# Kernel optimization log

Hardware: AMD Instinct MI355X
Metric: run time of the kernel (lower is better)

The kernel has to match this reference:

```python
import jax, jax.numpy as jnp
import numpy as np

H = 16  # num_heads
THETA = 10000.0


def apply_rope(x, positions, theta=THETA):
    # x: [..., S, d_k]; positions: [S]
    d_k = x.shape[-1]
    inv_freq = theta ** (-jnp.arange(0, d_k, 2, dtype=jnp.float32) / d_k)  # [d_k/2]
    ang = positions.astype(jnp.float32)[:, None] * inv_freq[None, :]  # [S, d_k/2]
    cos, sin = jnp.cos(ang), jnp.sin(ang)
    x1 = x[..., 0::2]
    x2 = x[..., 1::2]
    out_even = x1 * cos - x2 * sin
    out_odd = x1 * sin + x2 * cos
    out = jnp.stack([out_even, out_odd], axis=-1)  # [..., S, d_k/2, 2]
    return out.reshape(x.shape)


def setup_inputs() -> dict:
    key = jax.random.key(0)
    k1, k2, k3 = jax.random.split(key, 3)
    B, S, D = 2, 2048, 1024
    x = jax.random.normal(k1, (B, S, D), dtype=jnp.float32)
    token_positions = jnp.arange(S, dtype=jnp.int32)
    w_qkv = jax.random.normal(k2, (3 * D, D), dtype=jnp.float32) * (D ** -0.5)
    w_out = jax.random.normal(k3, (D, D), dtype=jnp.float32) * (D ** -0.5)
    return {"x": x, "token_positions": token_positions, "w_qkv": w_qkv, "w_out": w_out}


def reference(x, token_positions, w_qkv, w_out):
    B, S, D = x.shape
    d_k = D // H
    qkv = jnp.einsum('bsd,ed->bse', x, w_qkv)  # [B,S,3D]
    # split '(n h d_k)' -> n=3, h=H, d_k
    qkv = qkv.reshape(B, S, 3, H, d_k).transpose(2, 0, 3, 1, 4)  # [3,B,H,S,d_k]
    q = apply_rope(qkv[0], token_positions)
    k = apply_rope(qkv[1], token_positions)
    v = qkv[2]
    scale = 1.0 / jnp.sqrt(jnp.asarray(d_k, dtype=x.dtype))
    scores = jnp.einsum('bhqd,bhkd->bhqk', q, k) * scale  # [B,H,S,S]
    causal = jnp.tril(jnp.ones((S, S), dtype=bool))
    scores = jnp.where(causal, scores, jnp.asarray(-1e30, dtype=scores.dtype))
    attn = jax.nn.softmax(scores, axis=-1)
    out = jnp.einsum('bhqk,bhkd->bhqd', attn, v)  # [B,H,S,d_k]
    out = out.transpose(0, 2, 1, 3).reshape(B, S, D)  # merge (h d_v)
    return jnp.einsum('bsd,ed->bse', out, w_out)
```

## Files before the change

### kernel.cpp

```cpp
#include <hip/hip_runtime.h>

using bf16 = __bf16;
typedef __bf16 bf16x2 __attribute__((ext_vector_type(2)));
typedef __bf16 bf16x4v __attribute__((ext_vector_type(4)));
typedef __bf16 bf16x8 __attribute__((ext_vector_type(8)));
typedef float f32x4 __attribute__((ext_vector_type(4)));
typedef float floatx4 __attribute__((ext_vector_type(4)));

#define MFMA16(a, b, c) __builtin_amdgcn_mfma_f32_16x16x32_bf16((a), (b), (c), 0, 0, 0)

__device__ __forceinline__ float exp2a(float x) {
  float r;
  asm("v_exp_f32 %0, %1" : "=v"(r) : "v"(x));
  return r;
}

__global__ __launch_bounds__(256) void cast_kernel(const float* __restrict__ in,
                                                   bf16* __restrict__ out, int n4) {
  int i = blockIdx.x * 256 + threadIdx.x;
  if (i >= n4) return;
  floatx4 v = *(const floatx4*)(in + (size_t)i * 4);
  bf16x4v o;
  #pragma unroll
  for (int j = 0; j < 4; ++j) o[j] = (bf16)v[j];
  *(bf16x4v*)(out + (size_t)i * 4) = o;
}

template <bool OUT_F32>
__global__ __launch_bounds__(256, 2) void gemm_bt(const bf16* __restrict__ A,
                                                  const bf16* __restrict__ B,
                                                  void* __restrict__ Cv,
                                                  int M, int N, int K) {
  __shared__ bf16 As[128 * 32];
  __shared__ bf16 Bs[128 * 32];
  const int t = threadIdx.x;
  const int l = t & 63;
  const int w = t >> 6;
  const int m0 = blockIdx.y * 128;
  const int n0 = blockIdx.x * 128;
  const int wr = (w >> 1) * 64;
  const int wc = (w & 1) * 64;
  const int lr = l & 15;
  const int lk = (l >> 4) * 8;

  f32x4 acc[4][4] = {};

  const int srow = t >> 2;
  const int scol = (t & 3) * 8;

  for (int k0 = 0; k0 < K; k0 += 32) {
    __syncthreads();
    #pragma unroll
    for (int j = 0; j < 2; ++j) {
      const bf16* ga = A + (size_t)(m0 + j * 64 + srow) * K + k0 + scol;
      __builtin_amdgcn_global_load_lds(
          (const __attribute__((address_space(1))) void*)ga,
          (__attribute__((address_space(3))) void*)(As + (j * 64 + srow) * 32 + scol),
          16, 0, 0);
      const bf16* gb = B + (size_t)(n0 + j * 64 + srow) * K + k0 + scol;
      __builtin_amdgcn_global_load_lds(
          (const __attribute__((address_space(1))) void*)gb,
          (__attribute__((address_space(3))) void*)(Bs + (j * 64 + srow) * 32 + scol),
          16, 0, 0);
    }
    __syncthreads();
    bf16x8 af[4], bfr[4];
    #pragma unroll
    for (int i = 0; i < 4; ++i) af[i] = *(const bf16x8*)(As + (wr + i * 16 + lr) * 32 + lk);
    #pragma unroll
    for (int i = 0; i < 4; ++i) bfr[i] = *(const bf16x8*)(Bs + (wc + i * 16 + lr) * 32 + lk);
    #pragma unroll
    for (int i = 0; i < 4; ++i)
      #pragma unroll
      for (int j = 0; j < 4; ++j)
        acc[i][j] = MFMA16(af[i], bfr[j], acc[i][j]);
  }

  const int cr0 = (l >> 4) * 4;
  const int cc = l & 15;
  #pragma unroll
  for (int i = 0; i < 4; ++i) {
    #pragma unroll
    for (int j = 0; j < 4; ++j) {
      int row = m0 + wr + i * 16 + cr0;
      int col = n0 + wc + j * 16 + cc;
      #pragma unroll
      for (int r = 0; r < 4; ++r) {
        if constexpr (OUT_F32)
          ((float*)Cv)[(size_t)(row + r) * N + col] = acc[i][j][r];
        else
          ((bf16*)Cv)[(size_t)(row + r) * N + col] = (bf16)acc[i][j][r];
      }
    }
  }
}

__global__ __launch_bounds__(256) void rope_kernel(bf16* __restrict__ qkv,
                                                   const int* __restrict__ pos) {
  int idx = blockIdx.x * 256 + threadIdx.x;
  int i = idx & 31;
  int h = (idx >> 5) & 15;
  int row = idx >> 9;
  int s = row & 2047;
  float p = (float)pos[s];
  float freq = exp2f(-(float)i * (13.287712379549449f / 32.0f));
  float ang = p * freq;
  float sn, cs;
  sincosf(ang, &sn, &cs);
  size_t base = (size_t)row * 3072 + h * 64 + 2 * i;
  bf16x2 q = *(bf16x2*)(qkv + base);
  bf16x2 k = *(bf16x2*)(qkv + base + 1024);
  float q1 = (float)q[0], q2 = (float)q[1];
  float k1 = (float)k[0], k2 = (float)k[1];
  bf16x2 qo, ko;
  qo[0] = (bf16)(q1 * cs - q2 * sn);
  qo[1] = (bf16)(q1 * sn + q2 * cs);
  ko[0] = (bf16)(k1 * cs - k2 * sn);
  ko[1] = (bf16)(k1 * sn + k2 * cs);
  *(bf16x2*)(qkv + base) = qo;
  *(bf16x2*)(qkv + base + 1024) = ko;
}

__global__ __launch_bounds__(256, 4) void fa_causal(const bf16* __restrict__ qkv,
                                                    bf16* __restrict__ attn) {
  const int bh = blockIdx.x;
  const int b = bh >> 4, h = bh & 15;
  const int q0 = ((int)gridDim.y - 1 - (int)blockIdx.y) * 64;
  const int t = threadIdx.x, w = t >> 6, l = t & 63;
  const int lq = l & 15;
  const int g = l >> 4;
  const int lk = g * 8;
  const int swz = lq & 7;
  const int hz = lq >> 3;

  __shared__ bf16 Ks[2][64 * 64];
  __shared__ bf16 Vt[2][64 * 64];

  const size_t rs = 3072;
  const bf16* Qg = qkv + (size_t)(b * 2048) * rs + h * 64;
  const bf16* Kg = Qg + 1024;
  const bf16* Vg = Qg + 2048;

  const int qrow0 = q0 + w * 16;
  const int qg = qrow0 + lq;

  const float SC = 0.125f * 1.44269504088896f;
  bf16x8 qfr[2];
  #pragma unroll
  for (int kk = 0; kk < 2; ++kk) {
    bf16x8 qv = *(const bf16x8*)(Qg + (size_t)qg * rs + kk * 32 + lk);
    #pragma unroll
    for (int j = 0; j < 8; ++j) qv[j] = (bf16)((float)qv[j] * SC);
    qfr[kk] = qv;
  }

  f32x4 o[4] = {};
  float mrow = -1e30f, lrow = 0.f;

  const int nkt = (q0 + 64) >> 6;
  const int krow_in = l >> 3;
  const int kcsrc = (l & 7) ^ krow_in;
  const int kp = t >> 3;
  const int K0 = kp * 2;
  const int cd = t & 7;
  const int slot0 = (K0 & 32) | (((K0 >> 2) & 3) << 3) | (((K0 >> 4) & 1) << 2) | (K0 & 3);

  bf16x8 va, vb2;

  #define STAGE_K(KT, BUF)                                                                \
    {                                                                                     \
      _Pragma("unroll")                                                                   \
      for (int c = 0; c < 2; ++c) {                                                       \
        const int rowbase = w * 8 + c * 32;                                               \
        const bf16* src = Kg + (size_t)((KT)*64 + rowbase + krow_in) * rs + kcsrc * 8;    \
        __builtin_amdgcn_global_load_lds(                                                 \
            (const __attribute__((address_space(1))) void*)src,                           \
            (__attribute__((address_space(3))) void*)(&Ks[BUF][rowbase * 64]), 16, 0, 0); \
      }                                                                                   \
    }
  #define LOAD_V(KT)                                                          \
    {                                                                         \
      const bf16* vsrc = Vg + (size_t)((KT)*64 + K0) * rs + cd * 8;           \
      va = *(const bf16x8*)(vsrc);                                            \
      vb2 = *(const bf16x8*)(vsrc + rs);                                      \
    }
  #define WRITE_V(BUF)                                                        \
    {                                                                         \
      _Pragma("unroll")                                                       \
      for (int e = 0; e < 8; ++e) {                                           \
        bf16x2 pr;                                                            \
        pr[0] = va[e];                                                        \
        pr[1] = vb2[e];                                                       \
        *(bf16x2*)(&Vt[BUF][(cd * 8 + e) * 64 + (slot0 ^ ((e ^ cd) << 3))]) = pr; \
      }                                                                       \
    }

  STAGE_K(0, 0)
  LOAD_V(0)
  WRITE_V(0)
  __syncthreads();

  for (int kt = 0; kt < nkt; ++kt) {
    const bool pf = (kt + 1 < nkt);
    if (pf) {
      LOAD_V(kt + 1)
      STAGE_K(kt + 1, (kt + 1) & 1)
    }

    if (kt * 64 <= qrow0 + 15) {
      const bf16* Kc = Ks[kt & 1];
      const bf16* Vc = Vt[kt & 1];
      const bool fullw = (kt * 64 + 63 <= qrow0);

      f32x4 sc[4] = {};
      __builtin_amdgcn_s_setprio(1);
      #pragma unroll
      for (int kf = 0; kf < 4; ++kf) {
        const int krow = kf * 16 + lq;
        bf16x8 kb0 = *(const bf16x8*)(&Kc[krow * 64 + ((0 + g) ^ swz) * 8]);
        bf16x8 kb1 = *(const bf16x8*)(&Kc[krow * 64 + ((4 + g) ^ swz) * 8]);
        sc[kf] = MFMA16(kb0, qfr[0], sc[kf]);
        sc[kf] = MFMA16(kb1, qfr[1], sc[kf]);
      }
      __builtin_amdgcn_s_setprio(0);

      float pv[16];
      if (fullw) {
        #pragma unroll
        for (int i = 0; i < 16; ++i) pv[i] = sc[i >> 2][i & 3];
      } else {
        #pragma unroll
        for (int kf = 0; kf < 4; ++kf)
          #pragma unroll
          for (int r = 0; r < 4; ++r) {
            int key = kt * 64 + kf * 16 + g * 4 + r;
            pv[kf * 4 + r] = (key <= qg) ? sc[kf][r] : -1e30f;
          }
      }
      float mxl = fmaxf(fmaxf(pv[0], pv[1]), pv[2]);
      mxl = fmaxf(fmaxf(mxl, pv[3]), pv[4]);
      mxl = fmaxf(fmaxf(mxl, pv[5]), pv[6]);
      mxl = fmaxf(fmaxf(mxl, pv[7]), pv[8]);
      mxl = fmaxf(fmaxf(mxl, pv[9]), pv[10]);
      mxl = fmaxf(fmaxf(mxl, pv[11]), pv[12]);
      mxl = fmaxf(fmaxf(mxl, pv[13]), pv[14]);
      mxl = fmaxf(mxl, pv[15]);
      if (!__all(mxl <= mrow)) {
        float mx = fmaxf(mxl, __shfl_xor(mxl, 16, 64));
        mx = fmaxf(mx, __shfl_xor(mx, 32, 64));
        float mnew = fmaxf(mrow, mx);
        float al = exp2a(mrow - mnew);
        lrow *= al;
        #pragma unroll
        for (int fd = 0; fd < 4; ++fd)
          #pragma unroll
          for (int r = 0; r < 4; ++r) o[fd][r] *= al;
        mrow = mnew;
      }
      float rsum = 0.f;
      #pragma unroll
      for (int i = 0; i < 16; ++i) {
        float p = exp2a(pv[i] - mrow);
        pv[i] = p;
        rsum += p;
      }
      rsum += __shfl_xor(rsum, 16, 64);
      rsum += __shfl_xor(rsum, 32, 64);
      lrow += rsum;

      bf16x8 p0, p1;
      #pragma unroll
      for (int i = 0; i < 8; ++i) {
        p0[i] = (bf16)pv[i];
        p1[i] = (bf16)pv[8 + i];
      }

      __builtin_amdgcn_s_setprio(1);
      #pragma unroll
      for (int fd = 0; fd < 4; ++fd) {
        const int drow = fd * 16 + lq;
        {
          int pc = (0 * 4 + g) ^ swz ^ (fd << 1) ^ hz;
          bf16x8 vb = *(const bf16x8*)(&Vc[drow * 64 + pc * 8]);
          o[fd] = MFMA16(vb, p0, o[fd]);
        }
        {
          int pc = (1 * 4 + g) ^ swz ^ (fd << 1) ^ hz;
          bf16x8 vb = *(const bf16x8*)(&Vc[drow * 64 + pc * 8]);
          o[fd] = MFMA16(vb, p1, o[fd]);
        }
      }
      __builtin_amdgcn_s_setprio(0);
    }

    if (pf) {
      WRITE_V((kt + 1) & 1)
      __syncthreads();
    }
  }

  __syncthreads();
  bf16* Os = (bf16*)Ks + w * (16 * 72);
  float inv = 1.0f / lrow;
  #pragma unroll
  for (int fd = 0; fd < 4; ++fd) {
    bf16x4v ov;
    #pragma unroll
    for (int r = 0; r < 4; ++r) ov[r] = (bf16)(o[fd][r] * inv);
    *(bf16x4v*)(&Os[lq * 72 + fd * 16 + g * 4]) = ov;
  }
  asm volatile("" ::: "memory");
  #pragma unroll
  for (int p = 0; p < 2; ++p) {
    int idx = p * 64 + l;
    int row16 = idx >> 3, c8 = idx & 7;
    bf16x8 v = *(const bf16x8*)(&Os[row16 * 72 + c8 * 8]);
    *(bf16x8*)(&attn[(size_t)(b * 2048 + qrow0 + row16) * 1024 + h * 64 + c8 * 8]) = v;
  }
}

extern "C" void kernel_launch(void* const* d_in, const int* in_sizes, int n_in,
                              void* d_out, int out_size, void* d_ws, size_t ws_size,
                              hipStream_t stream) {
  const float* x = (const float*)d_in[0];
  const int* pos = (const int*)d_in[1];
  const float* w_qkv = (const float*)d_in[2];
  const float* w_out = (const float*)d_in[3];
  float* out = (float*)d_out;

  char* ws = (char*)d_ws;
  bf16* xb   = (bf16*)(ws);
  bf16* wqb  = (bf16*)(ws + (8u << 20));
  bf16* wob  = (bf16*)(ws + (14u << 20));
  bf16* qkv  = (bf16*)(ws + (16u << 20));
  bf16* attn = (bf16*)(ws + (40u << 20));

  cast_kernel<<<4096, 256, 0, stream>>>(x, xb, 4194304 / 4);
  cast_kernel<<<3072, 256, 0, stream>>>(w_qkv, wqb, 3145728 / 4);
  cast_kernel<<<1024, 256, 0, stream>>>(w_out, wob, 1048576 / 4);

  dim3 g1(3072 / 128, 4096 / 128);
  gemm_bt<false><<<g1, 256, 0, stream>>>(xb, wqb, (void*)qkv, 4096, 3072, 1024);

  rope_kernel<<<8192, 256, 0, stream>>>(qkv, pos);

  dim3 gfa(32, 2048 / 64);
  fa_causal<<<gfa, 256, 0, stream>>>(qkv, attn);

  dim3 g2(1024 / 128, 4096 / 128);
  gemm_bt<true><<<g2, 256, 0, stream>>>(attn, wob, (void*)out, 4096, 1024, 1024);
}
```

Measured before the change: 124.5 us.

## Fuse RoPE into QKV GEMM epilogue and merge three cast kernels

Removes the standalone RoPE kernel by applying the rotation in the QKV GEMM epilogue for Q and K columns. Each lane gets its pair partner with a lane xor-shuffle and computes sin/cos with the hardware v_sin/v_cos instructions on a range-reduced angle. The three fp32-to-bf16 cast launches become one kernel that branches by index. This saves a full read/write pass over Q and K and two launches, at the cost of extra epilogue work and lower-precision hardware trig.

```diff
diff --git a/kernel.cpp b/kernel.cpp
--- a/kernel.cpp
+++ b/kernel.cpp
@@ -15,22 +15,36 @@
   return r;
 }
 
-__global__ __launch_bounds__(256) void cast_kernel(const float* __restrict__ in,
-                                                   bf16* __restrict__ out, int n4) {
+__global__ __launch_bounds__(256) void cast3_kernel(const float* __restrict__ a,
+                                                    const float* __restrict__ b,
+                                                    const float* __restrict__ c,
+                                                    bf16* __restrict__ oa,
+                                                    bf16* __restrict__ ob,
+                                                    bf16* __restrict__ oc) {
   int i = blockIdx.x * 256 + threadIdx.x;
-  if (i >= n4) return;
-  floatx4 v = *(const floatx4*)(in + (size_t)i * 4);
+  const float* in;
+  bf16* out;
+  int off;
+  if (i < 1048576) {
+    in = a; out = oa; off = i;
+  } else if (i < 1835008) {
+    in = b; out = ob; off = i - 1048576;
+  } else {
+    in = c; out = oc; off = i - 1835008;
+  }
+  floatx4 v = *(const floatx4*)(in + (size_t)off * 4);
   bf16x4v o;
   #pragma unroll
   for (int j = 0; j < 4; ++j) o[j] = (bf16)v[j];
-  *(bf16x4v*)(out + (size_t)i * 4) = o;
-}
-
-template <bool OUT_F32>
+  *(bf16x4v*)(out + (size_t)off * 4) = o;
+}
+
+template <bool OUT_F32, bool ROPE>
 __global__ __launch_bounds__(256, 2) void gemm_bt(const bf16* __restrict__ A,
                                                   const bf16* __restrict__ B,
                                                   void* __restrict__ Cv,
-                                                  int M, int N, int K) {
+                                                  int M, int N, int K,
+                                                  const int* __restrict__ pos) {
   __shared__ bf16 As[128 * 32];
   __shared__ bf16 Bs[128 * 32];
   const int t = threadIdx.x;
@@ -78,6 +92,41 @@
 
   const int cr0 = (l >> 4) * 4;
   const int cc = l & 15;
+
+  if constexpr (ROPE) {
+    if (n0 < 2048) {
+      const float L2T32 = 13.287712379549449f / 32.0f;
+      const float INV2PI = 0.15915494309189535f;
+      float frev[4];
+      #pragma unroll
+      for (int j = 0; j < 4; ++j) {
+        int col = n0 + wc + j * 16 + cc;
+        int ip = (col & 63) >> 1;
+        frev[j] = exp2f(-(float)ip * L2T32) * INV2PI;
+      }
+      const float sgn = (cc & 1) ? 1.f : -1.f;
+      #pragma unroll
+      for (int i = 0; i < 4; ++i) {
+        #pragma unroll
+        for (int r = 0; r < 4; ++r) {
+          int row = m0 + wr + i * 16 + cr0 + r;
+          float p = (float)pos[row & 2047];
+          #pragma unroll
+          for (int j = 0; j < 4; ++j) {
+            float self = acc[i][j][r];
+            float partner = __shfl_xor(self, 1, 64);
+            float ang = p * frev[j];
+            float fr = ang - floorf(ang);
+            float sn, cs;
+            asm("v_sin_f32 %0, %1" : "=v"(sn) : "v"(fr));
+            asm("v_cos_f32 %0, %1" : "=v"(cs) : "v"(fr));
+            acc[i][j][r] = self * cs + sgn * sn * partner;
+          }
+        }
+      }
+    }
+  }
+
   #pragma unroll
   for (int i = 0; i < 4; ++i) {
     #pragma unroll
@@ -93,32 +142,6 @@
       }
     }
   }
-}
-
-__global__ __launch_bounds__(256) void rope_kernel(bf16* __restrict__ qkv,
-                                                   const int* __restrict__ pos) {
-  int idx = blockIdx.x * 256 + threadIdx.x;
-  int i = idx & 31;
-  int h = (idx >> 5) & 15;
-  int row = idx >> 9;
-  int s = row & 2047;
-  float p = (float)pos[s];
-  float freq = exp2f(-(float)i * (13.287712379549449f / 32.0f));
-  float ang = p * freq;
-  float sn, cs;
-  sincosf(ang, &sn, &cs);
-  size_t base = (size_t)row * 3072 + h * 64 + 2 * i;
-  bf16x2 q = *(bf16x2*)(qkv + base);
-  bf16x2 k = *(bf16x2*)(qkv + base + 1024);
-  float q1 = (float)q[0], q2 = (float)q[1];
-  float k1 = (float)k[0], k2 = (float)k[1];
-  bf16x2 qo, ko;
-  qo[0] = (bf16)(q1 * cs - q2 * sn);
-  qo[1] = (bf16)(q1 * sn + q2 * cs);
-  ko[0] = (bf16)(k1 * cs - k2 * sn);
-  ko[1] = (bf16)(k1 * sn + k2 * cs);
-  *(bf16x2*)(qkv + base) = qo;
-  *(bf16x2*)(qkv + base + 1024) = ko;
 }
 
 __global__ __launch_bounds__(256, 4) void fa_causal(const bf16* __restrict__ qkv,
@@ -335,18 +358,14 @@
   bf16* qkv  = (bf16*)(ws + (16u << 20));
   bf16* attn = (bf16*)(ws + (40u << 20));
 
-  cast_kernel<<<4096, 256, 0, stream>>>(x, xb, 4194304 / 4);
-  cast_kernel<<<3072, 256, 0, stream>>>(w_qkv, wqb, 3145728 / 4);
-  cast_kernel<<<1024, 256, 0, stream>>>(w_out, wob, 1048576 / 4);
+  cast3_kernel<<<8192, 256, 0, stream>>>(x, w_qkv, w_out, xb, wqb, wob);
 
   dim3 g1(3072 / 128, 4096 / 128);
-  gemm_bt<false><<<g1, 256, 0, stream>>>(xb, wqb, (void*)qkv, 4096, 3072, 1024);
-
-  rope_kernel<<<8192, 256, 0, stream>>>(qkv, pos);
+  gemm_bt<false, true><<<g1, 256, 0, stream>>>(xb, wqb, (void*)qkv, 4096, 3072, 1024, pos);
 
   dim3 gfa(32, 2048 / 64);
   fa_causal<<<gfa, 256, 0, stream>>>(qkv, attn);
 
   dim3 g2(1024 / 128, 4096 / 128);
-  gemm_bt<true><<<g2, 256, 0, stream>>>(attn, wob, (void*)out, 4096, 1024, 1024);
-}
+  gemm_bt<true, false><<<g2, 256, 0, stream>>>(attn, wob, (void*)out, 4096, 1024, 1024, nullptr);
+}
```

New measurement: 114.6 us, median of 2. -8.0%, faster.
